# Kernel tuning notes

Hardware: AMD Instinct MI355X
Metric: run time of the kernel (lower is better)

Reference implementation:

```python
import jax, jax.numpy as jnp
import numpy as np
import math

N, J = 8192, 22  # N = batch*frames (per-frame calls are independent), J = num_joint


def _layernorm(x, g, b, eps=1e-5):
    m = jnp.mean(x, axis=-1, keepdims=True)
    v = jnp.var(x, axis=-1, keepdims=True)
    return (x - m) * jax.lax.rsqrt(v + eps) * g + b


def _attention(x, Wqkv, bqkv, Wo, bo, heads):
    # x: [B, n, d]; matches torch Attention (scale = d**-0.5)
    B, n, d = x.shape
    hd = d // heads
    qkv = (x @ Wqkv + bqkv).reshape(B, n, 3, heads, hd).transpose(2, 0, 3, 1, 4)
    q, k, v = qkv[0], qkv[1], qkv[2]  # [B, h, n, hd]
    dots = jnp.einsum('bhid,bhjd->bhij', q, k) * (d ** -0.5)
    attn = jax.nn.softmax(dots, axis=-1)
    out = jnp.einsum('bhij,bhjd->bhid', attn, v)
    out = out.transpose(0, 2, 1, 3).reshape(B, n, -1)
    return out @ Wo + bo


def _encoder(x, tok_W, tok_b, qkv_W, qkv_b, o_W, o_b, ln_g, ln_b, m1_W, m1_b, m2_W, m2_b, heads):
    tok = x @ tok_W + tok_b                                   # [B, J, 64]
    h = _attention(tok, qkv_W, qkv_b, o_W, o_b, heads)        # [B, J, out_dim]
    hn = _layernorm(h, ln_g, ln_b)
    mlp = jax.nn.relu(hn @ m1_W + m1_b) @ m2_W + m2_b
    return h + mlp                                            # Residual(LN+MLP)


def _sinusoidal_pe(max_len, dim):
    pos = np.arange(max_len)[:, None].astype(np.float32)
    div = np.exp(np.arange(0, dim, 2, dtype=np.float32) * (-math.log(10000.0) / dim))
    pe = np.zeros((max_len, dim), dtype=np.float32)
    pe[:, 0::2] = np.sin(pos * div)
    pe[:, 1::2] = np.cos(pos * div)
    return jnp.asarray(pe)


def setup_inputs() -> dict:
    key = jax.random.key(0)
    ks = iter(jax.random.split(key, 64))
    rn = lambda shape, s=0.1: jax.random.normal(next(ks), shape, dtype=jnp.float32) * s
    inp = {
        'q_t': jax.random.normal(next(ks), (N, J, 4), dtype=jnp.float32),
        'skelA': jax.random.normal(next(ks), (N, J, 3), dtype=jnp.float32),
        'skelB': jax.random.normal(next(ks), (N, J, 3), dtype=jnp.float32),
        'quat_mean': jax.random.normal(next(ks), (J, 4), dtype=jnp.float32) * 0.1,
        'quat_std': jax.random.uniform(next(ks), (J, 4), dtype=jnp.float32, minval=0.5, maxval=1.5),
        # QuatEncoder params
        'qe_tok_W': rn((4, 64)), 'qe_tok_b': jnp.zeros((64,), jnp.float32),
        'qe_qkv_W': rn((64, 192)), 'qe_qkv_b': jnp.zeros((192,), jnp.float32),
        'qe_o_W': rn((64, 256)), 'qe_o_b': jnp.zeros((256,), jnp.float32),
        'qe_ln_g': jnp.ones((256,), jnp.float32), 'qe_ln_b': jnp.zeros((256,), jnp.float32),
        'qe_m1_W': rn((256, 512)), 'qe_m1_b': jnp.zeros((512,), jnp.float32),
        'qe_m2_W': rn((512, 256)), 'qe_m2_b': jnp.zeros((256,), jnp.float32),
        # shared SeklEncoder params
        'se_tok_W': rn((3, 64)), 'se_tok_b': jnp.zeros((64,), jnp.float32),
        'se_qkv_W': rn((64, 192)), 'se_qkv_b': jnp.zeros((192,), jnp.float32),
        'se_o_W': rn((64, 128)), 'se_o_b': jnp.zeros((128,), jnp.float32),
        'se_ln_g': jnp.ones((128,), jnp.float32), 'se_ln_b': jnp.zeros((128,), jnp.float32),
        'se_m1_W': rn((128, 256)), 'se_m1_b': jnp.zeros((256,), jnp.float32),
        'se_m2_W': rn((256, 128)), 'se_m2_b': jnp.zeros((128,), jnp.float32),
        # head
        'emb_W': rn((512, 128)), 'emb_b': jnp.zeros((128,), jnp.float32),
        'del_W': rn((128, 4)), 'del_b': jnp.zeros((4,), jnp.float32),
    }
    return inp


def reference(q_t, skelA, skelB, quat_mean, quat_std,
              qe_tok_W, qe_tok_b, qe_qkv_W, qe_qkv_b, qe_o_W, qe_o_b,
              qe_ln_g, qe_ln_b, qe_m1_W, qe_m1_b, qe_m2_W, qe_m2_b,
              se_tok_W, se_tok_b, se_qkv_W, se_qkv_b, se_o_W, se_o_b,
              se_ln_g, se_ln_b, se_m1_W, se_m1_b, se_m2_W, se_m2_b,
              emb_W, emb_b, del_W, del_b):
    q_embed = _encoder(q_t, qe_tok_W, qe_tok_b, qe_qkv_W, qe_qkv_b, qe_o_W, qe_o_b,
                       qe_ln_g, qe_ln_b, qe_m1_W, qe_m1_b, qe_m2_W, qe_m2_b, heads=4)   # [N,J,256]
    sA = _encoder(skelA, se_tok_W, se_tok_b, se_qkv_W, se_qkv_b, se_o_W, se_o_b,
                  se_ln_g, se_ln_b, se_m1_W, se_m1_b, se_m2_W, se_m2_b, heads=2)        # [N,J,128]
    sB = _encoder(skelB, se_tok_W, se_tok_b, se_qkv_W, se_qkv_b, se_o_W, se_o_b,
                  se_ln_g, se_ln_b, se_m1_W, se_m1_b, se_m2_W, se_m2_b, heads=2)        # [N,J,128]
    cat = jnp.concatenate([q_embed, sA, sB], axis=-1)                                   # [N,J,512]
    dim = cat.shape[-1]
    pe = _sinusoidal_pe(J, dim)
    pos = cat * math.sqrt(dim) + pe[None, :, :]
    embed = jax.nn.relu(pos @ emb_W + emb_b)                                            # [N,J,128]
    delta = embed @ del_W + del_b                                                       # [N,J,4]
    delta = delta * quat_std + quat_mean
    # normalized()
    lengths = jnp.sqrt(jnp.sum(delta * delta, axis=-1, keepdims=True))
    return delta / lengths
```

## Files before the change

kernel.cpp:

```cpp
#include <hip/hip_runtime.h>
#include <hip/hip_bf16.h>
#include <math.h>

#define NJ 22
#define MROWS 44
#define PROWS 48
#define NRT 3

typedef float f4 __attribute__((ext_vector_type(4)));
typedef _Float16 h8 __attribute__((ext_vector_type(8)));

#define WOFF_QE_QKV 0
#define WOFF_QE_O   24576
#define WOFF_QE_M1  57344
#define WOFF_QE_M2  319488
#define WOFF_SE_QKV 581632
#define WOFF_SE_O   606208
#define WOFF_SE_M1  622592
#define WOFF_SE_M2  688128
#define WOFF_EMB    753664
#define W_TOTAL     884736

struct Smem {
    _Float16 XH[PROWS * 256];
    __align__(16) char U[PROWS * 128 * 4];
    float LNp[PROWS * 4], LNq[PROWS * 4];
    float LNm[PROWS], LNr[PROWS];
    float Sx[MROWS * 4];
};

struct Args {
    const float *q_t, *skelA, *skelB, *quat_mean, *quat_std;
    const float *qe_tok_W, *qe_tok_b, *qe_qkv_b, *qe_o_b, *qe_ln_g, *qe_ln_b, *qe_m1_b, *qe_m2_b;
    const float *se_tok_W, *se_tok_b, *se_qkv_b, *se_o_b, *se_ln_g, *se_ln_b, *se_m1_b, *se_m2_b;
    const float *del_W, *del_b;
    const float *P;
    const _Float16 *W;
    _Float16 *cat;
    float *out;
};

__device__ __forceinline__ int swz(int r, int c) {
    return (((c >> 3) ^ (r & 7)) << 3) | (c & 7);
}

template<int NI, int KSTEPS, int LDA>
__device__ __forceinline__ void mfma_gemm(f4 (&acc)[NI][NRT],
        const _Float16 *AH,
        const _Float16 *BH, const _Float16 *BL,
        int wK, int koff, int w, int l) {
    const int m = l & 15, q = l >> 4;
#pragma unroll 1
    for (int s = 0; s < KSTEPS; s++) {
        const int ka = s * 32 + q * 8;
        h8 a[NRT];
#pragma unroll
        for (int rt = 0; rt < NRT; rt++) {
            int r = rt * 16 + m;
            a[rt] = *(const h8 *)(AH + r * LDA + (((ka >> 3) ^ (r & 7)) << 3));
        }
#pragma unroll
        for (int i = 0; i < NI; i++) {
            int n = (w + 4 * i) * 16 + m;
            int boff = n * wK + koff + ka;
            h8 bh = *(const h8 *)(BH + boff);
            h8 bl = *(const h8 *)(BL + boff);
#pragma unroll
            for (int rt = 0; rt < NRT; rt++) {
                acc[i][rt] = __builtin_amdgcn_mfma_f32_16x16x32_f16(a[rt], bh, acc[i][rt], 0, 0, 0);
                acc[i][rt] = __builtin_amdgcn_mfma_f32_16x16x32_f16(a[rt], bl, acc[i][rt], 0, 0, 0);
            }
        }
    }
}

template<int NH, int HD>
__device__ __forceinline__ void attention(Smem &sm, int t) {
    constexpr int SPL = HD / 16;
    if (t < NH * MROWS * SPL) {
        const int half = t & (SPL - 1);
        const int ur = t / SPL;
        const int hh = ur / MROWS;
        const int rr = ur - hh * MROWS;
        const int jb = (rr >= NJ) ? NJ : 0;
        const float *KF = (const float *)sm.U;
        const float *VF = KF + PROWS * 64;
        const int c0 = 64 + hh * HD + half * 16;
        float qv[16];
#pragma unroll
        for (int g = 0; g < 2; g++) {
            h8 qh = *(const h8 *)(sm.XH + rr * 256 + swz(rr, c0 + g * 8));
#pragma unroll
            for (int d = 0; d < 8; d++) qv[g * 8 + d] = (float)qh[d];
        }
        float s[NJ];
        float mx = -1e30f;
#pragma unroll
        for (int j = 0; j < NJ; j++) {
            const float *kp = KF + (jb + j) * 64 + hh * HD + half * 16;
            float acc = 0.f;
#pragma unroll
            for (int d = 0; d < 16; d += 4) {
                float4 v = *(const float4 *)(kp + d);
                acc += qv[d] * v.x + qv[d + 1] * v.y + qv[d + 2] * v.z + qv[d + 3] * v.w;
            }
            if constexpr (SPL == 2) acc += __shfl_xor(acc, 1);
            s[j] = acc * 0.125f;
            mx = fmaxf(mx, s[j]);
        }
        float sum = 0.f;
#pragma unroll
        for (int j = 0; j < NJ; j++) { s[j] = __expf(s[j] - mx); sum += s[j]; }
        float inv = 1.f / sum;
        float o[16];
#pragma unroll
        for (int d = 0; d < 16; d++) o[d] = 0.f;
#pragma unroll
        for (int j = 0; j < NJ; j++) {
            float p = s[j] * inv;
            const float *vp = VF + (jb + j) * 64 + hh * HD + half * 16;
#pragma unroll
            for (int d = 0; d < 16; d += 4) {
                float4 v = *(const float4 *)(vp + d);
                o[d] = fmaf(p, v.x, o[d]);       o[d + 1] = fmaf(p, v.y, o[d + 1]);
                o[d + 2] = fmaf(p, v.z, o[d + 2]); o[d + 3] = fmaf(p, v.w, o[d + 3]);
            }
        }
        const int cw = hh * HD + half * 16;
#pragma unroll
        for (int g = 0; g < 2; g++) {
            h8 oh;
#pragma unroll
            for (int d = 0; d < 8; d++) oh[d] = (_Float16)o[g * 8 + d];
            *(h8 *)(sm.XH + rr * 256 + swz(rr, cw + g * 8)) = oh;
        }
    }
}

template<int D, int NH, int TK>
__device__ __forceinline__ void encode(Smem &sm, const float *__restrict__ xg,
        const float *__restrict__ tokW, const float *__restrict__ tokB,
        const float *__restrict__ qkvB, const float *__restrict__ oB,
        const float *__restrict__ lnG,  const float *__restrict__ lnB,
        const float *__restrict__ m1B,  const float *__restrict__ m2B,
        const _Float16 *__restrict__ Wq,  const _Float16 *__restrict__ Wo,
        const _Float16 *__restrict__ Wm1, const _Float16 *__restrict__ Wm2,
        _Float16 *__restrict__ catb, int catoff, int t, int w, int l) {
    constexpr int NI = D / 64;
    constexpr int HID = 2 * D;
    const int m = l & 15, q = l >> 4;

    if (t < MROWS * TK) sm.Sx[t] = xg[t];
    __syncthreads();
    {
        float b = tokB[l];
#pragma unroll
        for (int i = 0; i < 11; i++) {
            int r = w + 4 * i;
            float acc = b;
#pragma unroll
            for (int k = 0; k < TK; k++)
                acc = fmaf(sm.Sx[r * TK + k], tokW[k * 64 + l], acc);
            sm.XH[r * 256 + swz(r, l)] = (_Float16)acc;
        }
    }
    __syncthreads();
    {
        f4 acc[3][NRT];
#pragma unroll
        for (int i = 0; i < 3; i++)
#pragma unroll
            for (int rt = 0; rt < NRT; rt++) acc[i][rt] = (f4){0.f, 0.f, 0.f, 0.f};
        mfma_gemm<3, 2, 256>(acc, sm.XH, Wq, Wq + 192 * 64, 64, 0, w, l);
        float *KV = (float *)sm.U;
#pragma unroll
        for (int i = 0; i < 3; i++) {
            int c = (w + 4 * i) * 16 + m;
            float b = qkvB[c];
#pragma unroll
            for (int rt = 0; rt < NRT; rt++)
#pragma unroll
                for (int e = 0; e < 4; e++) {
                    int r = rt * 16 + q * 4 + e;
                    float v = acc[i][rt][e] + b;
                    sm.XH[r * 256 + swz(r, 64 + c)] = (_Float16)v;
                    if (c >= 128)      KV[PROWS * 64 + r * 64 + (c - 128)] = v;
                    else if (c >= 64)  KV[r * 64 + (c - 64)] = v;
                }
        }
    }
    __syncthreads();
    attention<NH, 64 / NH>(sm, t);
    __syncthreads();
    f4 res[NI][NRT];
#pragma unroll
    for (int i = 0; i < NI; i++)
#pragma unroll
        for (int rt = 0; rt < NRT; rt++) res[i][rt] = (f4){0.f, 0.f, 0.f, 0.f};
    mfma_gemm<NI, 2, 256>(res, sm.XH, Wo, Wo + D * 64, 64, 0, w, l);
#pragma unroll
    for (int i = 0; i < NI; i++) {
        float b = oB[(w + 4 * i) * 16 + m];
#pragma unroll
        for (int rt = 0; rt < NRT; rt++)
#pragma unroll
            for (int e = 0; e < 4; e++) res[i][rt][e] += b;
    }
#pragma unroll
    for (int rt = 0; rt < NRT; rt++)
#pragma unroll
        for (int e = 0; e < 4; e++) {
            int r = rt * 16 + q * 4 + e;
            float s1 = 0.f, s2 = 0.f;
#pragma unroll
            for (int i = 0; i < NI; i++) {
                float v = res[i][rt][e];
                s1 += v; s2 = fmaf(v, v, s2);
            }
#pragma unroll
            for (int off = 8; off > 0; off >>= 1) {
                s1 += __shfl_xor(s1, off);
                s2 += __shfl_xor(s2, off);
            }
            if (m == 0) { sm.LNp[r * 4 + w] = s1; sm.LNq[r * 4 + w] = s2; }
        }
    __syncthreads();
    if (t < PROWS) {
        float s1 = sm.LNp[t * 4] + sm.LNp[t * 4 + 1] + sm.LNp[t * 4 + 2] + sm.LNp[t * 4 + 3];
        float s2 = sm.LNq[t * 4] + sm.LNq[t * 4 + 1] + sm.LNq[t * 4 + 2] + sm.LNq[t * 4 + 3];
        float mean = s1 * (1.f / D);
        float var = s2 * (1.f / D) - mean * mean;
        sm.LNm[t] = mean;
        sm.LNr[t] = rsqrtf(fmaxf(var, 0.f) + 1e-5f);
    }
    __syncthreads();
#pragma unroll
    for (int i = 0; i < NI; i++) {
        int c = (w + 4 * i) * 16 + m;
        float g = lnG[c], bb = lnB[c];
#pragma unroll
        for (int rt = 0; rt < NRT; rt++)
#pragma unroll
            for (int e = 0; e < 4; e++) {
                int r = rt * 16 + q * 4 + e;
                float v = (res[i][rt][e] - sm.LNm[r]) * sm.LNr[r] * g + bb;
                sm.XH[r * 256 + swz(r, c)] = (_Float16)v;
            }
    }
    __syncthreads();
    _Float16 *HH = (_Float16 *)sm.U;
#pragma unroll 1
    for (int cb = 0; cb < HID / 128; cb++) {
        f4 h1[2][NRT];
#pragma unroll
        for (int i = 0; i < 2; i++)
#pragma unroll
            for (int rt = 0; rt < NRT; rt++) h1[i][rt] = (f4){0.f, 0.f, 0.f, 0.f};
        mfma_gemm<2, D / 32, 256>(h1, sm.XH,
                                  Wm1 + cb * 128 * D, Wm1 + HID * D + cb * 128 * D, D, 0, w, l);
        __syncthreads();
#pragma unroll
        for (int i = 0; i < 2; i++) {
            int c = (w + 4 * i) * 16 + m;
            float b = m1B[cb * 128 + c];
#pragma unroll
            for (int rt = 0; rt < NRT; rt++)
#pragma unroll
                for (int e = 0; e < 4; e++) {
                    int r = rt * 16 + q * 4 + e;
                    HH[r * 128 + swz(r, c)] = (_Float16)fmaxf(h1[i][rt][e] + b, 0.f);
                }
        }
        __syncthreads();
        mfma_gemm<NI, 4, 128>(res, HH, Wm2, Wm2 + D * HID, HID, cb * 128, w, l);
    }
#pragma unroll
    for (int i = 0; i < NI; i++) {
        int c = (w + 4 * i) * 16 + m;
        float b = m2B[c];
#pragma unroll
        for (int rt = 0; rt < NRT; rt++)
#pragma unroll
            for (int e = 0; e < 4; e++) {
                int r = rt * 16 + q * 4 + e;
                if (r < MROWS)
                    catb[r * 512 + catoff + c] = (_Float16)(res[i][rt][e] + b);
            }
    }
}

__global__ __launch_bounds__(256, 2) void fused_kernel(Args A) {
    __shared__ __align__(16) Smem sm;
    const int t = threadIdx.x, w = t >> 6, l = t & 63;
    const int blk = blockIdx.x;

    for (int i = t; i < 4 * 256; i += 256) {
        int r = MROWS + (i >> 8), c = i & 255;
        sm.XH[r * 256 + c] = (_Float16)0.f;
    }

    const _Float16 *W = A.W;
    _Float16 *catb = A.cat + (size_t)blk * MROWS * 512;

    encode<256, 4, 4>(sm, A.q_t + blk * MROWS * 4,
                      A.qe_tok_W, A.qe_tok_b, A.qe_qkv_b, A.qe_o_b,
                      A.qe_ln_g, A.qe_ln_b, A.qe_m1_b, A.qe_m2_b,
                      W + WOFF_QE_QKV, W + WOFF_QE_O, W + WOFF_QE_M1, W + WOFF_QE_M2,
                      catb, 0, t, w, l);
    encode<128, 2, 3>(sm, A.skelA + blk * MROWS * 3,
                      A.se_tok_W, A.se_tok_b, A.se_qkv_b, A.se_o_b,
                      A.se_ln_g, A.se_ln_b, A.se_m1_b, A.se_m2_b,
                      W + WOFF_SE_QKV, W + WOFF_SE_O, W + WOFF_SE_M1, W + WOFF_SE_M2,
                      catb, 256, t, w, l);
    encode<128, 2, 3>(sm, A.skelB + blk * MROWS * 3,
                      A.se_tok_W, A.se_tok_b, A.se_qkv_b, A.se_o_b,
                      A.se_ln_g, A.se_ln_b, A.se_m1_b, A.se_m2_b,
                      W + WOFF_SE_QKV, W + WOFF_SE_O, W + WOFF_SE_M1, W + WOFF_SE_M2,
                      catb, 384, t, w, l);
}

struct HeadArgs {
    const _Float16 *cat;
    const _Float16 *W;
    const float *P;
    const float *del_W, *del_b, *quat_mean, *quat_std;
    float *out;
    int R;
};

#define ELD 132

__global__ __launch_bounds__(256, 4) void head_kernel(HeadArgs A) {
    __shared__ float E[64 * ELD];
    __shared__ float Sd[64 * 4];
    const int t = threadIdx.x, w = t >> 6, l = t & 63;
    const int m = l & 15, q = l >> 4;
    const int rowbase = blockIdx.x * 64;
    const _Float16 *BH = A.W + WOFF_EMB;
    const _Float16 *BL = BH + 128 * 512;

    f4 acc[2][4];
#pragma unroll
    for (int i = 0; i < 2; i++)
#pragma unroll
        for (int rt = 0; rt < 4; rt++) acc[i][rt] = (f4){0.f, 0.f, 0.f, 0.f};

#pragma unroll 1
    for (int s = 0; s < 16; s++) {
        const int ka = s * 32 + q * 8;
        h8 a[4];
#pragma unroll
        for (int rt = 0; rt < 4; rt++) {
            int rg = rowbase + rt * 16 + m;
            rg = rg < A.R ? rg : A.R - 1;
            a[rt] = *(const h8 *)(A.cat + (size_t)rg * 512 + ka);
        }
#pragma unroll
        for (int i = 0; i < 2; i++) {
            int n = (w + 4 * i) * 16 + m;
            h8 bh = *(const h8 *)(BH + n * 512 + ka);
            h8 bl = *(const h8 *)(BL + n * 512 + ka);
#pragma unroll
            for (int rt = 0; rt < 4; rt++) {
                acc[i][rt] = __builtin_amdgcn_mfma_f32_16x16x32_f16(a[rt], bh, acc[i][rt], 0, 0, 0);
                acc[i][rt] = __builtin_amdgcn_mfma_f32_16x16x32_f16(a[rt], bl, acc[i][rt], 0, 0, 0);
            }
        }
    }
#pragma unroll
    for (int i = 0; i < 2; i++) {
        int c = (w + 4 * i) * 16 + m;
#pragma unroll
        for (int rt = 0; rt < 4; rt++)
#pragma unroll
            for (int e = 0; e < 4; e++) {
                int r = rt * 16 + q * 4 + e;
                int j = (rowbase + r) % NJ;
                float v = fmaf(22.627416997969522f, acc[i][rt][e], A.P[j * 128 + c]);
                E[r * ELD + c] = fmaxf(v, 0.f);
            }
    }
    __syncthreads();
    {
        int r = t >> 2, d = t & 3;
        float a2 = A.del_b[d];
        const float *Er = E + r * ELD;
#pragma unroll 4
        for (int c4 = 0; c4 < 32; c4++) {
            float4 ev = *(const float4 *)(Er + c4 * 4);
            a2 = fmaf(ev.x, A.del_W[(c4 * 4 + 0) * 4 + d], a2);
            a2 = fmaf(ev.y, A.del_W[(c4 * 4 + 1) * 4 + d], a2);
            a2 = fmaf(ev.z, A.del_W[(c4 * 4 + 2) * 4 + d], a2);
            a2 = fmaf(ev.w, A.del_W[(c4 * 4 + 3) * 4 + d], a2);
        }
        int j = (rowbase + r) % NJ;
        Sd[t] = fmaf(a2, A.quat_std[j * 4 + d], A.quat_mean[j * 4 + d]);
    }
    __syncthreads();
    {
        int r = t >> 2;
        int rg = rowbase + r;
        if (rg < A.R) {
            float x0 = Sd[r * 4], x1 = Sd[r * 4 + 1];
            float x2 = Sd[r * 4 + 2], x3 = Sd[r * 4 + 3];
            float inv = 1.f / sqrtf(x0 * x0 + x1 * x1 + x2 * x2 + x3 * x3);
            A.out[(size_t)rg * 4 + (t & 3)] = Sd[t] * inv;
        }
    }
}

struct WDesc { const float *W; int K; int N; int off; };
struct SplitArgs { WDesc d[9]; _Float16 *out; };

__global__ void split_kernel(SplitArgs a) {
    WDesc d = a.d[blockIdx.y];
    int e = blockIdx.x * 256 + threadIdx.x;
    int tot = d.K * d.N;
    if (e < tot) {
        int n = e / d.K, k = e - n * d.K;
        float v = d.W[k * d.N + n];
        _Float16 h = (_Float16)v;
        a.out[d.off + e] = h;
        a.out[d.off + tot + e] = (_Float16)(v - (float)h);
    }
}

__global__ void pe_emb_kernel(const float *__restrict__ emb_W,
                              const float *__restrict__ emb_b, float *P) {
    int r = blockIdx.x;
    int c = threadIdx.x;
    float acc = emb_b[c];
    const float k = -2.f * logf(10000.f) / 512.f;
    for (int i = 0; i < 256; i++) {
        float ang = (float)r * expf((float)i * k);
        acc = fmaf(sinf(ang), emb_W[(2 * i) * 128 + c], acc);
        acc = fmaf(cosf(ang), emb_W[(2 * i + 1) * 128 + c], acc);
    }
    P[r * 128 + c] = acc;
}

extern "C" void kernel_launch(void *const *d_in, const int *in_sizes, int n_in,
                              void *d_out, int out_size, void *d_ws, size_t ws_size,
                              hipStream_t stream) {
    const float **in = (const float **)d_in;
    float *P = (float *)d_ws;
    _Float16 *W = (_Float16 *)((float *)d_ws + 22 * 128);
    _Float16 *cat = W + W_TOTAL;

    Args A;
    A.q_t = in[0]; A.skelA = in[1]; A.skelB = in[2]; A.quat_mean = in[3]; A.quat_std = in[4];
    A.qe_tok_W = in[5]; A.qe_tok_b = in[6]; A.qe_qkv_b = in[8]; A.qe_o_b = in[10];
    A.qe_ln_g = in[11]; A.qe_ln_b = in[12]; A.qe_m1_b = in[14]; A.qe_m2_b = in[16];
    A.se_tok_W = in[17]; A.se_tok_b = in[18]; A.se_qkv_b = in[20]; A.se_o_b = in[22];
    A.se_ln_g = in[23]; A.se_ln_b = in[24]; A.se_m1_b = in[26]; A.se_m2_b = in[28];
    A.del_W = in[31]; A.del_b = in[32];
    A.P = P; A.W = W; A.cat = cat; A.out = (float *)d_out;

    SplitArgs sa;
    sa.d[0] = { in[7],  64, 192, WOFF_QE_QKV };
    sa.d[1] = { in[9],  64, 256, WOFF_QE_O };
    sa.d[2] = { in[13], 256, 512, WOFF_QE_M1 };
    sa.d[3] = { in[15], 512, 256, WOFF_QE_M2 };
    sa.d[4] = { in[19], 64, 192, WOFF_SE_QKV };
    sa.d[5] = { in[21], 64, 128, WOFF_SE_O };
    sa.d[6] = { in[25], 128, 256, WOFF_SE_M1 };
    sa.d[7] = { in[27], 256, 128, WOFF_SE_M2 };
    sa.d[8] = { in[29], 512, 128, WOFF_EMB };
    sa.out = W;

    int n_items = in_sizes[0] / (NJ * 4);
    int blocks = n_items / 2;
    int R = n_items * NJ;

    HeadArgs H;
    H.cat = cat; H.W = W; H.P = P;
    H.del_W = in[31]; H.del_b = in[32]; H.quat_mean = in[3]; H.quat_std = in[4];
    H.out = (float *)d_out; H.R = R;

    split_kernel<<<dim3(512, 9), 256, 0, stream>>>(sa);
    pe_emb_kernel<<<NJ, 128, 0, stream>>>(in[29], in[30], P);
    fused_kernel<<<blocks, 256, 0, stream>>>(A);
    head_kernel<<<(R + 63) / 64, 256, 0, stream>>>(H);
}
```

Before: 1.383 ms.

## Process one item per block in fused kernel and software-pipeline head GEMM loads

The fused encoder kernel now handles one 22-row item per block instead of two (44 rows), shrinking shared memory and row tiles from three to two MFMA tiles. This allows three blocks per CU and removes the per-row key offset in attention. In exchange, padding rises from 4 to 10 rows out of 32, so more MFMA work is wasted, and the block count doubles. Separately, the head kernel's K loop is double-buffered so the next step's global loads are issued before the current step's MFMAs.

Result: slower. 2.275 ms (+64.5%).

```diff
diff --git a/kernel.cpp b/kernel.cpp
--- a/kernel.cpp
+++ b/kernel.cpp
@@ -3,9 +3,9 @@
 #include <math.h>
 
 #define NJ 22
-#define MROWS 44
-#define PROWS 48
-#define NRT 3
+#define MROWS 22
+#define PROWS 32
+#define NRT 2
 
 typedef float f4 __attribute__((ext_vector_type(4)));
 typedef _Float16 h8 __attribute__((ext_vector_type(8)));
@@ -82,7 +82,6 @@
         const int ur = t / SPL;
         const int hh = ur / MROWS;
         const int rr = ur - hh * MROWS;
-        const int jb = (rr >= NJ) ? NJ : 0;
         const float *KF = (const float *)sm.U;
         const float *VF = KF + PROWS * 64;
         const int c0 = 64 + hh * HD + half * 16;
@@ -97,7 +96,7 @@
         float mx = -1e30f;
 #pragma unroll
         for (int j = 0; j < NJ; j++) {
-            const float *kp = KF + (jb + j) * 64 + hh * HD + half * 16;
+            const float *kp = KF + j * 64 + hh * HD + half * 16;
             float acc = 0.f;
 #pragma unroll
             for (int d = 0; d < 16; d += 4) {
@@ -118,7 +117,7 @@
 #pragma unroll
         for (int j = 0; j < NJ; j++) {
             float p = s[j] * inv;
-            const float *vp = VF + (jb + j) * 64 + hh * HD + half * 16;
+            const float *vp = VF + j * 64 + hh * HD + half * 16;
 #pragma unroll
             for (int d = 0; d < 16; d += 4) {
                 float4 v = *(const float4 *)(vp + d);
@@ -155,13 +154,15 @@
     {
         float b = tokB[l];
 #pragma unroll
-        for (int i = 0; i < 11; i++) {
+        for (int i = 0; i < 6; i++) {
             int r = w + 4 * i;
-            float acc = b;
-#pragma unroll
-            for (int k = 0; k < TK; k++)
-                acc = fmaf(sm.Sx[r * TK + k], tokW[k * 64 + l], acc);
-            sm.XH[r * 256 + swz(r, l)] = (_Float16)acc;
+            if (r < MROWS) {
+                float acc = b;
+#pragma unroll
+                for (int k = 0; k < TK; k++)
+                    acc = fmaf(sm.Sx[r * TK + k], tokW[k * 64 + l], acc);
+                sm.XH[r * 256 + swz(r, l)] = (_Float16)acc;
+            }
         }
     }
     __syncthreads();
@@ -289,12 +290,12 @@
     }
 }
 
-__global__ __launch_bounds__(256, 2) void fused_kernel(Args A) {
+__global__ __launch_bounds__(256, 3) void fused_kernel(Args A) {
     __shared__ __align__(16) Smem sm;
     const int t = threadIdx.x, w = t >> 6, l = t & 63;
     const int blk = blockIdx.x;
 
-    for (int i = t; i < 4 * 256; i += 256) {
+    for (int i = t; i < 10 * 256; i += 256) {
         int r = MROWS + (i >> 8), c = i & 255;
         sm.XH[r * 256 + c] = (_Float16)0.f;
     }
@@ -339,34 +340,56 @@
     const _Float16 *BH = A.W + WOFF_EMB;
     const _Float16 *BL = BH + 128 * 512;
 
+    const _Float16 *ap[4];
+#pragma unroll
+    for (int rt = 0; rt < 4; rt++) {
+        int rg = rowbase + rt * 16 + m;
+        rg = rg < A.R ? rg : A.R - 1;
+        ap[rt] = A.cat + (size_t)rg * 512 + q * 8;
+    }
+    const _Float16 *bp0 = BH + ((w + 0) * 16 + m) * 512 + q * 8;
+    const _Float16 *bp1 = BH + ((w + 4) * 16 + m) * 512 + q * 8;
+    const _Float16 *lp0 = BL + ((w + 0) * 16 + m) * 512 + q * 8;
+    const _Float16 *lp1 = BL + ((w + 4) * 16 + m) * 512 + q * 8;
+
     f4 acc[2][4];
 #pragma unroll
     for (int i = 0; i < 2; i++)
 #pragma unroll
         for (int rt = 0; rt < 4; rt++) acc[i][rt] = (f4){0.f, 0.f, 0.f, 0.f};
 
+    h8 aA[4], aB[4], bA[2], bB[2], lA[2], lB[2];
+
+#define HLOADS(av, bv, lv, S) do { \
+        av[0] = *(const h8 *)(ap[0] + (S) * 32); \
+        av[1] = *(const h8 *)(ap[1] + (S) * 32); \
+        av[2] = *(const h8 *)(ap[2] + (S) * 32); \
+        av[3] = *(const h8 *)(ap[3] + (S) * 32); \
+        bv[0] = *(const h8 *)(bp0 + (S) * 32); \
+        bv[1] = *(const h8 *)(bp1 + (S) * 32); \
+        lv[0] = *(const h8 *)(lp0 + (S) * 32); \
+        lv[1] = *(const h8 *)(lp1 + (S) * 32); \
+    } while (0)
+#define HMFMAS(av, bv, lv) do { \
+        _Pragma("unroll") \
+        for (int i = 0; i < 2; i++) { \
+            _Pragma("unroll") \
+            for (int rt = 0; rt < 4; rt++) { \
+                acc[i][rt] = __builtin_amdgcn_mfma_f32_16x16x32_f16(av[rt], i ? bv[1] : bv[0], acc[i][rt], 0, 0, 0); \
+                acc[i][rt] = __builtin_amdgcn_mfma_f32_16x16x32_f16(av[rt], i ? lv[1] : lv[0], acc[i][rt], 0, 0, 0); \
+            } \
+        } \
+    } while (0)
+
+    HLOADS(aA, bA, lA, 0);
 #pragma unroll 1
-    for (int s = 0; s < 16; s++) {
-        const int ka = s * 32 + q * 8;
-        h8 a[4];
-#pragma unroll
-        for (int rt = 0; rt < 4; rt++) {
-            int rg = rowbase + rt * 16 + m;
-            rg = rg < A.R ? rg : A.R - 1;
-            a[rt] = *(const h8 *)(A.cat + (size_t)rg * 512 + ka);
-        }
-#pragma unroll
-        for (int i = 0; i < 2; i++) {
-            int n = (w + 4 * i) * 16 + m;
-            h8 bh = *(const h8 *)(BH + n * 512 + ka);
-            h8 bl = *(const h8 *)(BL + n * 512 + ka);
-#pragma unroll
-            for (int rt = 0; rt < 4; rt++) {
-                acc[i][rt] = __builtin_amdgcn_mfma_f32_16x16x32_f16(a[rt], bh, acc[i][rt], 0, 0, 0);
-                acc[i][rt] = __builtin_amdgcn_mfma_f32_16x16x32_f16(a[rt], bl, acc[i][rt], 0, 0, 0);
-            }
-        }
-    }
+    for (int s = 0; s < 16; s += 2) {
+        HLOADS(aB, bB, lB, s + 1);
+        HMFMAS(aA, bA, lA);
+        if (s + 2 < 16) HLOADS(aA, bA, lA, s + 2);
+        HMFMAS(aB, bB, lB);
+    }
+
 #pragma unroll
     for (int i = 0; i < 2; i++) {
         int c = (w + 4 * i) * 16 + m;
@@ -469,7 +492,7 @@
     sa.out = W;
 
     int n_items = in_sizes[0] / (NJ * 4);
-    int blocks = n_items / 2;
+    int blocks = n_items;
     int R = n_items * NJ;
 
     HeadArgs H;
```

## Fold token projection into QKV weights and trim encoder barriers

Applied to the files above, without the earlier changes.

Precomputes the product of token and QKV weights (plus bias) in a small kernel, so each encoder computes Q/K/V directly from the 3–4 input features with FMAs instead of a token projection followed by an MFMA GEMM. LayerNorm statistics are now computed redundantly per thread to drop a barrier and shared arrays. The MLP hidden buffer is double-buffered to remove a sync per chunk, and the head kernel prefetches A operands one step ahead. Folding changes the rounding path slightly (fp32 folded weights instead of fp16 split GEMM) and adds one extra tiny launch.

Measured after the change: 1.303 ms. -5.8%, faster.

```diff
diff --git a/kernel.cpp b/kernel.cpp
--- a/kernel.cpp
+++ b/kernel.cpp
@@ -25,19 +25,16 @@
     _Float16 XH[PROWS * 256];
     __align__(16) char U[PROWS * 128 * 4];
     float LNp[PROWS * 4], LNq[PROWS * 4];
-    float LNm[PROWS], LNr[PROWS];
     float Sx[MROWS * 4];
 };
 
 struct Args {
-    const float *q_t, *skelA, *skelB, *quat_mean, *quat_std;
-    const float *qe_tok_W, *qe_tok_b, *qe_qkv_b, *qe_o_b, *qe_ln_g, *qe_ln_b, *qe_m1_b, *qe_m2_b;
-    const float *se_tok_W, *se_tok_b, *se_qkv_b, *se_o_b, *se_ln_g, *se_ln_b, *se_m1_b, *se_m2_b;
-    const float *del_W, *del_b;
-    const float *P;
+    const float *q_t, *skelA, *skelB;
+    const float *qe_o_b, *qe_ln_g, *qe_ln_b, *qe_m1_b, *qe_m2_b;
+    const float *se_o_b, *se_ln_g, *se_ln_b, *se_m1_b, *se_m2_b;
+    const float *fqe, *fse;
     const _Float16 *W;
     _Float16 *cat;
-    float *out;
 };
 
 __device__ __forceinline__ int swz(int r, int c) {
@@ -139,54 +136,41 @@
 
 template<int D, int NH, int TK>
 __device__ __forceinline__ void encode(Smem &sm, const float *__restrict__ xg,
-        const float *__restrict__ tokW, const float *__restrict__ tokB,
-        const float *__restrict__ qkvB, const float *__restrict__ oB,
+        const float *__restrict__ F,
+        const float *__restrict__ oB,
         const float *__restrict__ lnG,  const float *__restrict__ lnB,
         const float *__restrict__ m1B,  const float *__restrict__ m2B,
-        const _Float16 *__restrict__ Wq,  const _Float16 *__restrict__ Wo,
+        const _Float16 *__restrict__ Wo,
         const _Float16 *__restrict__ Wm1, const _Float16 *__restrict__ Wm2,
         _Float16 *__restrict__ catb, int catoff, int t, int w, int l) {
     constexpr int NI = D / 64;
     constexpr int HID = 2 * D;
     const int m = l & 15, q = l >> 4;
+    const float *FW = F, *Fb = F + TK * 192;
 
     if (t < MROWS * TK) sm.Sx[t] = xg[t];
     __syncthreads();
     {
-        float b = tokB[l];
+        float *KV = (float *)sm.U;
 #pragma unroll
         for (int i = 0; i < 11; i++) {
             int r = w + 4 * i;
-            float acc = b;
-#pragma unroll
-            for (int k = 0; k < TK; k++)
-                acc = fmaf(sm.Sx[r * TK + k], tokW[k * 64 + l], acc);
-            sm.XH[r * 256 + swz(r, l)] = (_Float16)acc;
-        }
-    }
-    __syncthreads();
-    {
-        f4 acc[3][NRT];
-#pragma unroll
-        for (int i = 0; i < 3; i++)
-#pragma unroll
-            for (int rt = 0; rt < NRT; rt++) acc[i][rt] = (f4){0.f, 0.f, 0.f, 0.f};
-        mfma_gemm<3, 2, 256>(acc, sm.XH, Wq, Wq + 192 * 64, 64, 0, w, l);
-        float *KV = (float *)sm.U;
-#pragma unroll
-        for (int i = 0; i < 3; i++) {
-            int c = (w + 4 * i) * 16 + m;
-            float b = qkvB[c];
-#pragma unroll
-            for (int rt = 0; rt < NRT; rt++)
-#pragma unroll
-                for (int e = 0; e < 4; e++) {
-                    int r = rt * 16 + q * 4 + e;
-                    float v = acc[i][rt][e] + b;
-                    sm.XH[r * 256 + swz(r, 64 + c)] = (_Float16)v;
-                    if (c >= 128)      KV[PROWS * 64 + r * 64 + (c - 128)] = v;
-                    else if (c >= 64)  KV[r * 64 + (c - 64)] = v;
-                }
+            float x0 = sm.Sx[r * TK + 0];
+            float x1 = sm.Sx[r * TK + 1];
+            float x2 = sm.Sx[r * TK + 2];
+            float x3 = (TK == 4) ? sm.Sx[r * TK + 3] : 0.f;
+#pragma unroll
+            for (int kk = 0; kk < 3; kk++) {
+                int c = kk * 64 + l;
+                float acc = Fb[c];
+                acc = fmaf(x0, FW[0 * 192 + c], acc);
+                acc = fmaf(x1, FW[1 * 192 + c], acc);
+                acc = fmaf(x2, FW[2 * 192 + c], acc);
+                if (TK == 4) acc = fmaf(x3, FW[3 * 192 + c], acc);
+                if (kk == 0)      sm.XH[r * 256 + swz(r, 64 + l)] = (_Float16)acc;
+                else if (kk == 1) KV[r * 64 + l] = acc;
+                else              KV[PROWS * 64 + r * 64 + l] = acc;
+            }
         }
     }
     __syncthreads();
@@ -225,30 +209,32 @@
             if (m == 0) { sm.LNp[r * 4 + w] = s1; sm.LNq[r * 4 + w] = s2; }
         }
     __syncthreads();
-    if (t < PROWS) {
-        float s1 = sm.LNp[t * 4] + sm.LNp[t * 4 + 1] + sm.LNp[t * 4 + 2] + sm.LNp[t * 4 + 3];
-        float s2 = sm.LNq[t * 4] + sm.LNq[t * 4 + 1] + sm.LNq[t * 4 + 2] + sm.LNq[t * 4 + 3];
-        float mean = s1 * (1.f / D);
-        float var = s2 * (1.f / D) - mean * mean;
-        sm.LNm[t] = mean;
-        sm.LNr[t] = rsqrtf(fmaxf(var, 0.f) + 1e-5f);
-    }
-    __syncthreads();
-#pragma unroll
-    for (int i = 0; i < NI; i++) {
-        int c = (w + 4 * i) * 16 + m;
-        float g = lnG[c], bb = lnB[c];
+    {
+        float gv[NI], bv[NI];
+#pragma unroll
+        for (int i = 0; i < NI; i++) {
+            int c = (w + 4 * i) * 16 + m;
+            gv[i] = lnG[c]; bv[i] = lnB[c];
+        }
 #pragma unroll
         for (int rt = 0; rt < NRT; rt++)
 #pragma unroll
             for (int e = 0; e < 4; e++) {
                 int r = rt * 16 + q * 4 + e;
-                float v = (res[i][rt][e] - sm.LNm[r]) * sm.LNr[r] * g + bb;
-                sm.XH[r * 256 + swz(r, c)] = (_Float16)v;
-            }
-    }
-    __syncthreads();
-    _Float16 *HH = (_Float16 *)sm.U;
+                float s1 = sm.LNp[r * 4] + sm.LNp[r * 4 + 1] + sm.LNp[r * 4 + 2] + sm.LNp[r * 4 + 3];
+                float s2 = sm.LNq[r * 4] + sm.LNq[r * 4 + 1] + sm.LNq[r * 4 + 2] + sm.LNq[r * 4 + 3];
+                float mean = s1 * (1.f / D);
+                float var = s2 * (1.f / D) - mean * mean;
+                float rinv = rsqrtf(fmaxf(var, 0.f) + 1e-5f);
+#pragma unroll
+                for (int i = 0; i < NI; i++) {
+                    int c = (w + 4 * i) * 16 + m;
+                    float v = (res[i][rt][e] - mean) * rinv * gv[i] + bv[i];
+                    sm.XH[r * 256 + swz(r, c)] = (_Float16)v;
+                }
+            }
+    }
+    __syncthreads();
 #pragma unroll 1
     for (int cb = 0; cb < HID / 128; cb++) {
         f4 h1[2][NRT];
@@ -258,7 +244,7 @@
             for (int rt = 0; rt < NRT; rt++) h1[i][rt] = (f4){0.f, 0.f, 0.f, 0.f};
         mfma_gemm<2, D / 32, 256>(h1, sm.XH,
                                   Wm1 + cb * 128 * D, Wm1 + HID * D + cb * 128 * D, D, 0, w, l);
-        __syncthreads();
+        _Float16 *HH = (_Float16 *)sm.U + (cb & 1) * (PROWS * 128);
 #pragma unroll
         for (int i = 0; i < 2; i++) {
             int c = (w + 4 * i) * 16 + m;
@@ -302,20 +288,17 @@
     const _Float16 *W = A.W;
     _Float16 *catb = A.cat + (size_t)blk * MROWS * 512;
 
-    encode<256, 4, 4>(sm, A.q_t + blk * MROWS * 4,
-                      A.qe_tok_W, A.qe_tok_b, A.qe_qkv_b, A.qe_o_b,
-                      A.qe_ln_g, A.qe_ln_b, A.qe_m1_b, A.qe_m2_b,
-                      W + WOFF_QE_QKV, W + WOFF_QE_O, W + WOFF_QE_M1, W + WOFF_QE_M2,
+    encode<256, 4, 4>(sm, A.q_t + blk * MROWS * 4, A.fqe,
+                      A.qe_o_b, A.qe_ln_g, A.qe_ln_b, A.qe_m1_b, A.qe_m2_b,
+                      W + WOFF_QE_O, W + WOFF_QE_M1, W + WOFF_QE_M2,
                       catb, 0, t, w, l);
-    encode<128, 2, 3>(sm, A.skelA + blk * MROWS * 3,
-                      A.se_tok_W, A.se_tok_b, A.se_qkv_b, A.se_o_b,
-                      A.se_ln_g, A.se_ln_b, A.se_m1_b, A.se_m2_b,
-                      W + WOFF_SE_QKV, W + WOFF_SE_O, W + WOFF_SE_M1, W + WOFF_SE_M2,
+    encode<128, 2, 3>(sm, A.skelA + blk * MROWS * 3, A.fse,
+                      A.se_o_b, A.se_ln_g, A.se_ln_b, A.se_m1_b, A.se_m2_b,
+                      W + WOFF_SE_O, W + WOFF_SE_M1, W + WOFF_SE_M2,
                       catb, 256, t, w, l);
-    encode<128, 2, 3>(sm, A.skelB + blk * MROWS * 3,
-                      A.se_tok_W, A.se_tok_b, A.se_qkv_b, A.se_o_b,
-                      A.se_ln_g, A.se_ln_b, A.se_m1_b, A.se_m2_b,
-                      W + WOFF_SE_QKV, W + WOFF_SE_O, W + WOFF_SE_M1, W + WOFF_SE_M2,
+    encode<128, 2, 3>(sm, A.skelB + blk * MROWS * 3, A.fse,
+                      A.se_o_b, A.se_ln_g, A.se_ln_b, A.se_m1_b, A.se_m2_b,
+                      W + WOFF_SE_O, W + WOFF_SE_M1, W + WOFF_SE_M2,
                       catb, 384, t, w, l);
 }
 
@@ -339,34 +322,59 @@
     const _Float16 *BH = A.W + WOFF_EMB;
     const _Float16 *BL = BH + 128 * 512;
 
+    const _Float16 *ap0, *ap1, *ap2, *ap3;
+    {
+        int r0 = rowbase + 0 * 16 + m; r0 = r0 < A.R ? r0 : A.R - 1;
+        int r1 = rowbase + 1 * 16 + m; r1 = r1 < A.R ? r1 : A.R - 1;
+        int r2 = rowbase + 2 * 16 + m; r2 = r2 < A.R ? r2 : A.R - 1;
+        int r3 = rowbase + 3 * 16 + m; r3 = r3 < A.R ? r3 : A.R - 1;
+        ap0 = A.cat + (size_t)r0 * 512 + q * 8;
+        ap1 = A.cat + (size_t)r1 * 512 + q * 8;
+        ap2 = A.cat + (size_t)r2 * 512 + q * 8;
+        ap3 = A.cat + (size_t)r3 * 512 + q * 8;
+    }
+    const _Float16 *bp0 = BH + ((w + 0) * 16 + m) * 512 + q * 8;
+    const _Float16 *bp1 = BH + ((w + 4) * 16 + m) * 512 + q * 8;
+    const _Float16 *lp0 = bp0 + 128 * 512;
+    const _Float16 *lp1 = bp1 + 128 * 512;
+
     f4 acc[2][4];
 #pragma unroll
     for (int i = 0; i < 2; i++)
 #pragma unroll
         for (int rt = 0; rt < 4; rt++) acc[i][rt] = (f4){0.f, 0.f, 0.f, 0.f};
 
+    h8 aA[4], aB[4];
+
+#define HA_LOAD(av, S) do { \
+        av[0] = *(const h8 *)(ap0 + (S) * 32); \
+        av[1] = *(const h8 *)(ap1 + (S) * 32); \
+        av[2] = *(const h8 *)(ap2 + (S) * 32); \
+        av[3] = *(const h8 *)(ap3 + (S) * 32); \
+    } while (0)
+#define H_STEP(av, S) do { \
+        h8 b0 = *(const h8 *)(bp0 + (S) * 32); \
+        h8 b1 = *(const h8 *)(bp1 + (S) * 32); \
+        h8 l0 = *(const h8 *)(lp0 + (S) * 32); \
+        h8 l1 = *(const h8 *)(lp1 + (S) * 32); \
+        _Pragma("unroll") \
+        for (int rt = 0; rt < 4; rt++) { \
+            acc[0][rt] = __builtin_amdgcn_mfma_f32_16x16x32_f16(av[rt], b0, acc[0][rt], 0, 0, 0); \
+            acc[0][rt] = __builtin_amdgcn_mfma_f32_16x16x32_f16(av[rt], l0, acc[0][rt], 0, 0, 0); \
+            acc[1][rt] = __builtin_amdgcn_mfma_f32_16x16x32_f16(av[rt], b1, acc[1][rt], 0, 0, 0); \
+            acc[1][rt] = __builtin_amdgcn_mfma_f32_16x16x32_f16(av[rt], l1, acc[1][rt], 0, 0, 0); \
+        } \
+    } while (0)
+
+    HA_LOAD(aA, 0);
 #pragma unroll 1
-    for (int s = 0; s < 16; s++) {
-        const int ka = s * 32 + q * 8;
-        h8 a[4];
-#pragma unroll
-        for (int rt = 0; rt < 4; rt++) {
-            int rg = rowbase + rt * 16 + m;
-            rg = rg < A.R ? rg : A.R - 1;
-            a[rt] = *(const h8 *)(A.cat + (size_t)rg * 512 + ka);
-        }
-#pragma unroll
-        for (int i = 0; i < 2; i++) {
-            int n = (w + 4 * i) * 16 + m;
-            h8 bh = *(const h8 *)(BH + n * 512 + ka);
-            h8 bl = *(const h8 *)(BL + n * 512 + ka);
-#pragma unroll
-            for (int rt = 0; rt < 4; rt++) {
-                acc[i][rt] = __builtin_amdgcn_mfma_f32_16x16x32_f16(a[rt], bh, acc[i][rt], 0, 0, 0);
-                acc[i][rt] = __builtin_amdgcn_mfma_f32_16x16x32_f16(a[rt], bl, acc[i][rt], 0, 0, 0);
-            }
-        }
-    }
+    for (int s = 0; s < 16; s += 2) {
+        HA_LOAD(aB, s + 1);
+        H_STEP(aA, s);
+        if (s + 2 < 16) HA_LOAD(aA, s + 2);
+        H_STEP(aB, s + 1);
+    }
+
 #pragma unroll
     for (int i = 0; i < 2; i++) {
         int c = (w + 4 * i) * 16 + m;
@@ -425,6 +433,41 @@
     }
 }
 
+struct FoldArgs {
+    const float *qe_tokW, *qe_tokB, *qe_qkvW, *qe_qkvB;
+    const float *se_tokW, *se_tokB, *se_qkvW, *se_qkvB;
+    float *fqe, *fse;
+};
+
+__global__ void fold_kernel(FoldArgs a) {
+    int c = threadIdx.x;
+    if (blockIdx.x == 0) {
+#pragma unroll
+        for (int kk = 0; kk < 4; kk++) {
+            float acc = 0.f;
+            for (int k = 0; k < 64; k++)
+                acc = fmaf(a.qe_tokW[kk * 64 + k], a.qe_qkvW[k * 192 + c], acc);
+            a.fqe[kk * 192 + c] = acc;
+        }
+        float acc = a.qe_qkvB[c];
+        for (int k = 0; k < 64; k++)
+            acc = fmaf(a.qe_tokB[k], a.qe_qkvW[k * 192 + c], acc);
+        a.fqe[4 * 192 + c] = acc;
+    } else {
+#pragma unroll
+        for (int kk = 0; kk < 3; kk++) {
+            float acc = 0.f;
+            for (int k = 0; k < 64; k++)
+                acc = fmaf(a.se_tokW[kk * 64 + k], a.se_qkvW[k * 192 + c], acc);
+            a.fse[kk * 192 + c] = acc;
+        }
+        float acc = a.se_qkvB[c];
+        for (int k = 0; k < 64; k++)
+            acc = fmaf(a.se_tokB[k], a.se_qkvW[k * 192 + c], acc);
+        a.fse[3 * 192 + c] = acc;
+    }
+}
+
 __global__ void pe_emb_kernel(const float *__restrict__ emb_W,
                               const float *__restrict__ emb_b, float *P) {
     int r = blockIdx.x;
@@ -443,18 +486,21 @@
                               void *d_out, int out_size, void *d_ws, size_t ws_size,
                               hipStream_t stream) {
     const float **in = (const float **)d_in;
-    float *P = (float *)d_ws;
-    _Float16 *W = (_Float16 *)((float *)d_ws + 22 * 128);
+    float *dwf = (float *)d_ws;
+    float *P   = dwf;
+    float *FQE = dwf + 2816;
+    float *FSE = dwf + 3776;
+    _Float16 *W = (_Float16 *)(dwf + 4544);
     _Float16 *cat = W + W_TOTAL;
 
     Args A;
-    A.q_t = in[0]; A.skelA = in[1]; A.skelB = in[2]; A.quat_mean = in[3]; A.quat_std = in[4];
-    A.qe_tok_W = in[5]; A.qe_tok_b = in[6]; A.qe_qkv_b = in[8]; A.qe_o_b = in[10];
-    A.qe_ln_g = in[11]; A.qe_ln_b = in[12]; A.qe_m1_b = in[14]; A.qe_m2_b = in[16];
-    A.se_tok_W = in[17]; A.se_tok_b = in[18]; A.se_qkv_b = in[20]; A.se_o_b = in[22];
-    A.se_ln_g = in[23]; A.se_ln_b = in[24]; A.se_m1_b = in[26]; A.se_m2_b = in[28];
-    A.del_W = in[31]; A.del_b = in[32];
-    A.P = P; A.W = W; A.cat = cat; A.out = (float *)d_out;
+    A.q_t = in[0]; A.skelA = in[1]; A.skelB = in[2];
+    A.qe_o_b = in[10]; A.qe_ln_g = in[11]; A.qe_ln_b = in[12];
+    A.qe_m1_b = in[14]; A.qe_m2_b = in[16];
+    A.se_o_b = in[22]; A.se_ln_g = in[23]; A.se_ln_b = in[24];
+    A.se_m1_b = in[26]; A.se_m2_b = in[28];
+    A.fqe = FQE; A.fse = FSE;
+    A.W = W; A.cat = cat;
 
     SplitArgs sa;
     sa.d[0] = { in[7],  64, 192, WOFF_QE_QKV };
@@ -468,6 +514,11 @@
     sa.d[8] = { in[29], 512, 128, WOFF_EMB };
     sa.out = W;
 
+    FoldArgs fa;
+    fa.qe_tokW = in[5];  fa.qe_tokB = in[6];  fa.qe_qkvW = in[7];  fa.qe_qkvB = in[8];
+    fa.se_tokW = in[17]; fa.se_tokB = in[18]; fa.se_qkvW = in[19]; fa.se_qkvB = in[20];
+    fa.fqe = FQE; fa.fse = FSE;
+
     int n_items = in_sizes[0] / (NJ * 4);
     int blocks = n_items / 2;
     int R = n_items * NJ;
@@ -478,6 +529,7 @@
     H.out = (float *)d_out; H.R = R;
 
     split_kernel<<<dim3(512, 9), 256, 0, stream>>>(sa);
+    fold_kernel<<<2, 192, 0, stream>>>(fa);
     pe_emb_kernel<<<NJ, 128, 0, stream>>>(in[29], in[30], P);
     fused_kernel<<<blocks, 256, 0, stream>>>(A);
     head_kernel<<<(R + 63) / 64, 256, 0, stream>>>(H);
```
